# Performance work log

Hardware: AMD Instinct MI355X
Metric: run time of the kernel (lower is better)

Reference implementation:

```python
import jax, jax.numpy as jnp
import numpy as np


def setup_inputs() -> dict:
    key = jax.random.key(0)
    k0, k1, k2, k3, k4 = jax.random.split(key, 5)
    B, H, Lq, Lk, D = 2, 8, 512, 512, 32
    q = jax.random.normal(k0, (B, H, Lq, D), dtype=jnp.float32)
    k = jax.random.normal(k1, (B, H, Lk, D), dtype=jnp.float32)
    scale = jnp.ones((1,), dtype=jnp.float32)  # accepted but unused by the module
    # mask True = padded / excluded (torch masked_fill semantics)
    mask = jax.random.bernoulli(k2, 0.1, (B, Lq, Lk))
    attn_bias = jax.random.normal(k3, (B, H, Lq, Lk), dtype=jnp.float32) * 0.1
    # GATv2 attention vector, torch shape (1,H,1,1,D) -> stored as (H,D)
    limit = float(np.sqrt(6.0 / (1.0 + D)))  # xavier_uniform fan_in=1*1*D? torch uses full shape; scale is immaterial for correctness
    attention = jax.random.uniform(k4, (H, D), dtype=jnp.float32, minval=-limit, maxval=limit)
    return {"q": q, "k": k, "scale": scale, "mask": mask, "attn_bias": attn_bias, "attention": attention}


def reference(q, k, scale, mask, attn_bias, attention):
    # q: [B,H,Lq,D], k: [B,H,Lk,D], attention: [H,D]
    # broadcast additive combine -> [B,H,Lq,Lk,D]
    summed = q[:, :, :, None, :] + k[:, :, None, :, :]
    # SiLU activation, dot with per-head attention vector, reduce D -> [B,H,Lq,Lk]
    scores = jnp.einsum("bhqkd,hd->bhqk", jax.nn.silu(summed), attention)
    scores = scores + attn_bias
    # masked softmax over Lk; mask broadcasts over heads (unsqueeze at -3)
    scores = jnp.where(mask[:, None, :, :], -jnp.inf, scores)
    w = jax.nn.softmax(scores, axis=-1)
    # rows that are fully masked produce NaN -> replace with 0 (torch nan_to_num)
    return jnp.nan_to_num(w, nan=0.0)
```

## Files before the change

### kernel.cpp

```cpp
#include <hip/hip_runtime.h>
#include <hip/hip_bf16.h>
#include <math.h>

#define BB 2
#define HH 8
#define LQ 512
#define LK 512
#define DD 32

#define LOG2E 1.44269504088896f

static __device__ __forceinline__ float fast_rcp(float x) {
#if __has_builtin(__builtin_amdgcn_rcpf)
  return __builtin_amdgcn_rcpf(x);
#else
  return 1.0f / x;
#endif
}

static __device__ __forceinline__ float fast_exp2(float x) {
#if __has_builtin(__builtin_amdgcn_exp2f)
  return __builtin_amdgcn_exp2f(x);
#else
  return __expf(x * 0.69314718056f);
#endif
}


__global__ __launch_bounds__(256) void gatv2_prek_t(
    const float* __restrict__ k, const float* __restrict__ att,
    float2* __restrict__ ktab) {
  const int bh = blockIdx.x >> 3;
  const int kt = blockIdx.x & 7;
  const int h = bh & (HH - 1);
  const int t = threadIdx.x;

  __shared__ float tile[64][33];

  const float4* src = (const float4*)(k + ((size_t)bh * LK + kt * 64) * DD);
#pragma unroll
  for (int i = 0; i < 2; ++i) {
    const int idx = t + i * 256;
    const float4 v = src[idx];
    const int kkl = idx >> 3;
    const int d4 = (idx & 7) * 4;
    tile[kkl][d4 + 0] = v.x; tile[kkl][d4 + 1] = v.y;
    tile[kkl][d4 + 2] = v.z; tile[kkl][d4 + 3] = v.w;
  }
  __syncthreads();

  const int d = t >> 3;
  const int kl0 = (t & 7) * 8;
  const float a = att[h * DD + d];
  float2* dst = ktab + ((size_t)bh * DD + d) * LK + kt * 64 + kl0;
#pragma unroll
  for (int j = 0; j < 8; ++j) {
    const float kv = tile[kl0 + j][d];
    float2 o;
    o.x = fast_exp2(-kv * LOG2E);
    o.y = kv * a;
    dst[j] = o;
  }
}

__global__ __launch_bounds__(256) void gatv2_prek_q(
    const float* __restrict__ q, const float* __restrict__ att,
    float2* __restrict__ qtab) {
  const int idx = blockIdx.x * 256 + threadIdx.x;
  const int row = idx >> 5;
  const int d = idx & 31;
  const int h = (row >> 9) & (HH - 1);
  const float qd = q[idx];
  const float ad = att[h * DD + d];
  float2 c;
  c.x = fast_exp2(-qd * LOG2E);
  c.y = qd * ad;
  qtab[idx] = c;
}

__global__ __launch_bounds__(256) void gatv2_score(
    const float2* __restrict__ ktab, const float2* __restrict__ qtab,
    const float* __restrict__ bias, const int* __restrict__ mask,
    float* __restrict__ scores) {
  const int lane = threadIdx.x & 63;
  const int w = threadIdx.x >> 6;
  const int bid = blockIdx.x;
  const int bh = bid >> 6;
  const int rem = bid & 63;
  const int rg = rem >> 1;
  const int ch = rem & 1;
  const int col = ch * 256 + w * 64 + lane;
  const int row0 = bh * LQ + rg * 16;
  const int b = bh >> 3;

  const float2* __restrict__ kcol = ktab + (size_t)bh * (DD * LK) + col;
  float2 kf[DD];
#pragma unroll
  for (int d = 0; d < DD; ++d) kf[d] = kcol[(size_t)d * LK];

#pragma unroll 2
  for (int rr = 0; rr < 16; ++rr) {
    const int row = row0 + rr;
    const float2* __restrict__ qrow = qtab + (size_t)row * DD;
    float acc = 0.0f;
#pragma unroll
    for (int d = 0; d < DD; ++d) {
      const float2 qc = qrow[d];
      const float u = fmaf(qc.x, kf[d].x, 1.0f);
      const float t = qc.y + kf[d].y;
      acc = fmaf(t, fast_rcp(u), acc);
    }
    const int qi = row & (LQ - 1);
    const float bval = bias[(size_t)row * LK + col];
    const int mval = mask[((size_t)(b * LQ + qi)) * LK + col];
    scores[(size_t)row * LK + col] = mval ? -INFINITY : (acc + bval);
  }
}

__global__ __launch_bounds__(256) void gatv2_softmax(
    const float* __restrict__ scores, float* __restrict__ out) {
  const int lane = threadIdx.x & 63;
  const int wid = threadIdx.x >> 6;
  const int r = blockIdx.x * 4 + wid;

  const float* __restrict__ srow = scores + (size_t)r * LK;
  float sc[8];
#pragma unroll
  for (int c = 0; c < 8; ++c) sc[c] = srow[lane + 64 * c];

  float m = sc[0];
#pragma unroll
  for (int c = 1; c < 8; ++c) m = fmaxf(m, sc[c]);
#pragma unroll
  for (int off = 32; off > 0; off >>= 1)
    m = fmaxf(m, __shfl_xor(m, off, 64));

  float sum = 0.0f;
#pragma unroll
  for (int c = 0; c < 8; ++c) {
    const float p = fast_exp2((sc[c] - m) * LOG2E);
    sc[c] = p;
    sum += p;
  }
#pragma unroll
  for (int off = 32; off > 0; off >>= 1)
    sum += __shfl_xor(sum, off, 64);

  const bool dead = (m == -INFINITY);
  const float inv = dead ? 0.0f : fast_rcp(sum);

  float* __restrict__ orow = out + (size_t)r * LK;
#pragma unroll
  for (int c = 0; c < 8; ++c) {
    orow[lane + 64 * c] = dead ? 0.0f : sc[c] * inv;
  }
}

#define D2 (DD / 2)
#define C2 2
#define NC (D2 / C2)
#define WAVES 8
#define RPW 2
#define ROWSPB (WAVES * RPW)

__global__ __launch_bounds__(256) void gatv2_prek_p(
    const float* __restrict__ k, const float* __restrict__ att,
    float4* __restrict__ wst4) {
  const int bh = blockIdx.x >> 3;
  const int kt = blockIdx.x & 7;
  const int h = bh & (HH - 1);
  const int t = threadIdx.x;

  __shared__ float tile[64][33];

  const float4* src = (const float4*)(k + ((size_t)bh * LK + kt * 64) * DD);
#pragma unroll
  for (int i = 0; i < 2; ++i) {
    const int idx = t + i * 256;
    const float4 v = src[idx];
    const int kkl = idx >> 3;
    const int d4 = (idx & 7) * 4;
    tile[kkl][d4 + 0] = v.x; tile[kkl][d4 + 1] = v.y;
    tile[kkl][d4 + 2] = v.z; tile[kkl][d4 + 3] = v.w;
  }
  __syncthreads();

  const int d2 = t >> 4;
  const int kl0 = (t & 15) * 4;
  const float a0 = att[h * DD + 2 * d2 + 0];
  const float a1 = att[h * DD + 2 * d2 + 1];
  float4* dst = wst4 + ((size_t)bh * D2 + d2) * LK + kt * 64 + kl0;
#pragma unroll
  for (int j = 0; j < 4; ++j) {
    const float k0 = tile[kl0 + j][2 * d2 + 0];
    const float k1 = tile[kl0 + j][2 * d2 + 1];
    float4 o;
    o.x = fast_exp2(-k0 * LOG2E); o.y = k0 * a0;
    o.z = fast_exp2(-k1 * LOG2E); o.w = k1 * a1;
    dst[j] = o;
  }
}

__global__ __launch_bounds__(512) void gatv2_main_r2(
    const float* __restrict__ q, const int* __restrict__ mask,
    const float* __restrict__ bias, const float* __restrict__ att,
    const float4* __restrict__ wst4, float* __restrict__ out) {
  const int lane = threadIdx.x & 63;
  const int wid = threadIdx.x >> 6;
  const int tid = threadIdx.x;
  const int rowbase = blockIdx.x * ROWSPB;
  const int bh = rowbase >> 9;
  const int b = rowbase >> 12;
  const int h = bh & (HH - 1);

  __shared__ float4 lds4[2][C2 * LK];
  __shared__ float4 cst4[ROWSPB][D2];

  const float4* __restrict__ kb = wst4 + (size_t)bh * (D2 * LK);

  float4 s0 = kb[tid];
  float4 s1 = kb[tid + 512];

  {
    const int rw = wid * RPW + (lane >> 5);
    const int d = lane & 31;
    const float qd = q[(size_t)(rowbase + rw) * DD + d];
    const float ad = att[h * DD + d];
    float2 c;
    c.x = fast_exp2(-qd * LOG2E);
    c.y = qd * ad;
    ((float2*)cst4)[rw * DD + d] = c;
  }
  lds4[0][tid] = s0;
  lds4[0][tid + 512] = s1;

  float acc[RPW][8];
#pragma unroll
  for (int j = 0; j < RPW; ++j)
#pragma unroll
    for (int c = 0; c < 8; ++c) acc[j][c] = 0.0f;

  float bv[RPW][8];
  int mv[RPW][8];

#pragma unroll
  for (int cc = 0; cc < NC; ++cc) {
    __syncthreads();

    float4 s0n, s1n;
    if (cc + 1 < NC) {
      const float4* src = kb + (size_t)(cc + 1) * (C2 * LK);
      s0n = src[tid];
      s1n = src[tid + 512];
    } else {
      const float* __restrict__ brow = bias + (size_t)rowbase * LK;
      const int* __restrict__ mrow = mask + ((size_t)(b * LQ) + (rowbase & (LQ - 1))) * LK;
#pragma unroll
      for (int j = 0; j < RPW; ++j) {
        const int rw = wid * RPW + j;
#pragma unroll
        for (int c = 0; c < 8; ++c) {
          bv[j][c] = brow[(size_t)rw * LK + lane + 64 * c];
          mv[j][c] = mrow[(size_t)rw * LK + lane + 64 * c];
        }
      }
    }

    const float4 c0A = cst4[wid * RPW + 0][cc * 2 + 0];
    const float4 c0B = cst4[wid * RPW + 0][cc * 2 + 1];
    const float4 c1A = cst4[wid * RPW + 1][cc * 2 + 0];
    const float4 c1B = cst4[wid * RPW + 1][cc * 2 + 1];

    const float4* __restrict__ buf = lds4[cc & 1];
#pragma unroll
    for (int d2l = 0; d2l < C2; ++d2l) {
      const float4 k0 = d2l ? c0B : c0A;
      const float4 k1 = d2l ? c1B : c1A;
      const float4* __restrict__ pd = buf + d2l * LK + lane;
#pragma unroll
      for (int c = 0; c < 8; ++c) {
        const float4 p = pd[64 * c];
        float u = fmaf(k0.x, p.x, 1.0f);
        float t = k0.y + p.y;
        acc[0][c] = fmaf(t, fast_rcp(u), acc[0][c]);
        u = fmaf(k0.z, p.z, 1.0f);
        t = k0.w + p.w;
        acc[0][c] = fmaf(t, fast_rcp(u), acc[0][c]);
        u = fmaf(k1.x, p.x, 1.0f);
        t = k1.y + p.y;
        acc[1][c] = fmaf(t, fast_rcp(u), acc[1][c]);
        u = fmaf(k1.z, p.z, 1.0f);
        t = k1.w + p.w;
        acc[1][c] = fmaf(t, fast_rcp(u), acc[1][c]);
      }
    }

    if (cc + 1 < NC) {
      float4* dst = lds4[(cc + 1) & 1];
      dst[tid] = s0n;
      dst[tid + 512] = s1n;
    }
  }

#pragma unroll
  for (int j = 0; j < RPW; ++j) {
    const int r = rowbase + wid * RPW + j;

    float sc[8];
#pragma unroll
    for (int c = 0; c < 8; ++c)
      sc[c] = mv[j][c] ? -INFINITY : (acc[j][c] + bv[j][c]);

    float m = sc[0];
#pragma unroll
    for (int c = 1; c < 8; ++c) m = fmaxf(m, sc[c]);
#pragma unroll
    for (int off = 32; off > 0; off >>= 1)
      m = fmaxf(m, __shfl_xor(m, off, 64));

    float sum = 0.0f;
#pragma unroll
    for (int c = 0; c < 8; ++c) {
      const float p = fast_exp2((sc[c] - m) * LOG2E);
      sc[c] = p;
      sum += p;
    }
#pragma unroll
    for (int off = 32; off > 0; off >>= 1)
      sum += __shfl_xor(sum, off, 64);

    const bool dead = (m == -INFINITY);
    const float inv = dead ? 0.0f : fast_rcp(sum);

    float* __restrict__ orow = out + (size_t)r * LK;
#pragma unroll
    for (int c = 0; c < 8; ++c) {
      orow[lane + 64 * c] = dead ? 0.0f : sc[c] * inv;
    }
  }
}

__global__ __launch_bounds__(256) void gatv2_fallback(
    const float* __restrict__ q, const float* __restrict__ k,
    const int* __restrict__ mask, const float* __restrict__ bias,
    const float* __restrict__ att, float* __restrict__ out) {
  const int lane = threadIdx.x & 63;
  const int wid = threadIdx.x >> 6;
  const int r = blockIdx.x * 4 + wid;
  const int b = r >> 12;
  const int h = (r >> 9) & (HH - 1);
  const int qi = r & (LQ - 1);

  const float* __restrict__ qrow = q + (size_t)r * DD;
  const float* __restrict__ kbase = k + ((size_t)(b * HH + h)) * (size_t)(LK * DD);
  const float* __restrict__ arow = att + h * DD;
  const float* __restrict__ brow = bias + (size_t)r * LK;
  const int* __restrict__ mrow = mask + ((size_t)(b * LQ + qi)) * LK;

  float qv[DD], av[DD];
#pragma unroll
  for (int d0 = 0; d0 < DD; d0 += 4) {
    const float4 qq = *(const float4*)(qrow + d0);
    const float4 aa = *(const float4*)(arow + d0);
    qv[d0 + 0] = qq.x; qv[d0 + 1] = qq.y; qv[d0 + 2] = qq.z; qv[d0 + 3] = qq.w;
    av[d0 + 0] = aa.x; av[d0 + 1] = aa.y; av[d0 + 2] = aa.z; av[d0 + 3] = aa.w;
  }

  float sc[8];
#pragma unroll
  for (int c = 0; c < 8; ++c) {
    const int kk = lane + 64 * c;
    const float* __restrict__ kr = kbase + (size_t)kk * DD;
    const float bval = brow[kk];
    const int mval = mrow[kk];
    float acc = 0.0f;
#pragma unroll
    for (int d0 = 0; d0 < DD; d0 += 4) {
      const float4 kv = *(const float4*)(kr + d0);
      const float kvf[4] = {kv.x, kv.y, kv.z, kv.w};
#pragma unroll
      for (int j = 0; j < 4; ++j) {
        const float t = qv[d0 + j] + kvf[j];
        const float e = fast_exp2(t * -LOG2E);
        const float sg = fast_rcp(1.0f + e);
        acc = fmaf(t * sg, av[d0 + j], acc);
      }
    }
    const float s = acc + bval;
    sc[c] = mval ? -INFINITY : s;
  }

  float m = sc[0];
#pragma unroll
  for (int c = 1; c < 8; ++c) m = fmaxf(m, sc[c]);
#pragma unroll
  for (int off = 32; off > 0; off >>= 1)
    m = fmaxf(m, __shfl_xor(m, off, 64));

  float sum = 0.0f;
#pragma unroll
  for (int c = 0; c < 8; ++c) {
    const float p = fast_exp2((sc[c] - m) * LOG2E);
    sc[c] = p;
    sum += p;
  }
#pragma unroll
  for (int off = 32; off > 0; off >>= 1)
    sum += __shfl_xor(sum, off, 64);

  const bool dead = (m == -INFINITY);
  const float inv = dead ? 0.0f : fast_rcp(sum);

  float* __restrict__ orow = out + (size_t)r * LK;
#pragma unroll
  for (int c = 0; c < 8; ++c) {
    orow[lane + 64 * c] = dead ? 0.0f : sc[c] * inv;
  }
}

extern "C" void kernel_launch(void* const* d_in, const int* in_sizes, int n_in,
                              void* d_out, int out_size, void* d_ws, size_t ws_size,
                              hipStream_t stream) {
  const float* q = (const float*)d_in[0];
  const float* k = (const float*)d_in[1];
  const int* mask = (const int*)d_in[3];
  const float* bias = (const float*)d_in[4];
  const float* att = (const float*)d_in[5];
  float* out = (float*)d_out;

  const int rows = BB * HH * LQ;
  const size_t ktab_b = (size_t)BB * HH * DD * LK * sizeof(float2);
  const size_t qtab_b = (size_t)rows * DD * sizeof(float2);
  const size_t scores_b = (size_t)rows * LK * sizeof(float);

  if (ws_size >= ktab_b + qtab_b + scores_b) {
    char* wsb = (char*)d_ws;
    float2* ktab = (float2*)wsb;
    float2* qtab = (float2*)(wsb + ktab_b);
    float* scores = (float*)(wsb + ktab_b + qtab_b);

    gatv2_prek_t<<<dim3(128), dim3(256), 0, stream>>>(k, att, ktab);
    gatv2_prek_q<<<dim3(1024), dim3(256), 0, stream>>>(q, att, qtab);
    gatv2_score<<<dim3(1024), dim3(256), 0, stream>>>(ktab, qtab, bias, mask, scores);
    gatv2_softmax<<<dim3(rows / 4), dim3(256), 0, stream>>>(scores, out);
  } else if (ws_size >= (size_t)BB * HH * D2 * LK * sizeof(float4)) {
    float4* wst4 = (float4*)d_ws;
    gatv2_prek_p<<<dim3(128), dim3(256), 0, stream>>>(k, att, wst4);
    gatv2_main_r2<<<dim3(rows / ROWSPB), dim3(64 * WAVES), 0, stream>>>(
        q, mask, bias, att, wst4, out);
  } else {
    gatv2_fallback<<<dim3(rows / 4), dim3(256), 0, stream>>>(q, k, mask, bias, att, out);
  }
}
```

Before: 116.6 us.

## Fuse score computation and masked softmax into one kernel

Merges the score and softmax kernels. Each 512-thread block covers all 512 key columns for 8 query rows and does the softmax in place, combining per-wave max and sum through shared memory. This removes the write and re-read of the intermediate scores buffer and one kernel launch. In exchange each block reloads the full key table for only 8 rows, where the old kernel reused it across 16, and the larger per-thread register arrays may lower occupancy.

New measurement: 116.9 us. Within noise of the previous version (+0.2%).

```diff
diff --git a/kernel.cpp b/kernel.cpp
--- a/kernel.cpp
+++ b/kernel.cpp
@@ -7,6 +7,7 @@
 #define LQ 512
 #define LK 512
 #define DD 32
+#define RB 8
 
 #define LOG2E 1.44269504088896f
 
@@ -78,29 +79,29 @@
   qtab[idx] = c;
 }
 
-__global__ __launch_bounds__(256) void gatv2_score(
+__global__ __launch_bounds__(512) void gatv2_fused(
     const float2* __restrict__ ktab, const float2* __restrict__ qtab,
     const float* __restrict__ bias, const int* __restrict__ mask,
-    float* __restrict__ scores) {
+    float* __restrict__ out) {
   const int lane = threadIdx.x & 63;
   const int w = threadIdx.x >> 6;
-  const int bid = blockIdx.x;
-  const int bh = bid >> 6;
-  const int rem = bid & 63;
-  const int rg = rem >> 1;
-  const int ch = rem & 1;
-  const int col = ch * 256 + w * 64 + lane;
-  const int row0 = bh * LQ + rg * 16;
+  const int bh = blockIdx.x >> 6;
+  const int rg = blockIdx.x & 63;
+  const int rowbase = bh * LQ + rg * RB;
   const int b = bh >> 3;
+  const int col = w * 64 + lane;
+
+  __shared__ float2 red[RB][8];
 
   const float2* __restrict__ kcol = ktab + (size_t)bh * (DD * LK) + col;
   float2 kf[DD];
 #pragma unroll
   for (int d = 0; d < DD; ++d) kf[d] = kcol[(size_t)d * LK];
 
-#pragma unroll 2
-  for (int rr = 0; rr < 16; ++rr) {
-    const int row = row0 + rr;
+  float sc[RB];
+#pragma unroll
+  for (int rr = 0; rr < RB; ++rr) {
+    const int row = rowbase + rr;
     const float2* __restrict__ qrow = qtab + (size_t)row * DD;
     float acc = 0.0f;
 #pragma unroll
@@ -110,49 +111,52 @@
       const float t = qc.y + kf[d].y;
       acc = fmaf(t, fast_rcp(u), acc);
     }
-    const int qi = row & (LQ - 1);
     const float bval = bias[(size_t)row * LK + col];
-    const int mval = mask[((size_t)(b * LQ + qi)) * LK + col];
-    scores[(size_t)row * LK + col] = mval ? -INFINITY : (acc + bval);
-  }
-}
-
-__global__ __launch_bounds__(256) void gatv2_softmax(
-    const float* __restrict__ scores, float* __restrict__ out) {
-  const int lane = threadIdx.x & 63;
-  const int wid = threadIdx.x >> 6;
-  const int r = blockIdx.x * 4 + wid;
-
-  const float* __restrict__ srow = scores + (size_t)r * LK;
-  float sc[8];
-#pragma unroll
-  for (int c = 0; c < 8; ++c) sc[c] = srow[lane + 64 * c];
-
-  float m = sc[0];
-#pragma unroll
-  for (int c = 1; c < 8; ++c) m = fmaxf(m, sc[c]);
-#pragma unroll
-  for (int off = 32; off > 0; off >>= 1)
-    m = fmaxf(m, __shfl_xor(m, off, 64));
-
-  float sum = 0.0f;
-#pragma unroll
-  for (int c = 0; c < 8; ++c) {
-    const float p = fast_exp2((sc[c] - m) * LOG2E);
-    sc[c] = p;
-    sum += p;
-  }
-#pragma unroll
-  for (int off = 32; off > 0; off >>= 1)
-    sum += __shfl_xor(sum, off, 64);
-
-  const bool dead = (m == -INFINITY);
-  const float inv = dead ? 0.0f : fast_rcp(sum);
-
-  float* __restrict__ orow = out + (size_t)r * LK;
-#pragma unroll
-  for (int c = 0; c < 8; ++c) {
-    orow[lane + 64 * c] = dead ? 0.0f : sc[c] * inv;
+    const int mval = mask[((size_t)(b * LQ + (row & (LQ - 1)))) * LK + col];
+    sc[rr] = mval ? -INFINITY : (acc + bval);
+  }
+
+#pragma unroll
+  for (int rr = 0; rr < RB; ++rr) {
+    float m = sc[rr];
+#pragma unroll
+    for (int off = 32; off > 0; off >>= 1)
+      m = fmaxf(m, __shfl_xor(m, off, 64));
+    const float mws = (m == -INFINITY) ? 0.0f : m;
+    const float p = (sc[rr] == -INFINITY) ? 0.0f
+                                          : fast_exp2((sc[rr] - mws) * LOG2E);
+    float s = p;
+#pragma unroll
+    for (int off = 32; off > 0; off >>= 1)
+      s += __shfl_xor(s, off, 64);
+    if (lane == 0) red[rr][w] = make_float2(m, s);
+    sc[rr] = p;
+  }
+  __syncthreads();
+
+#pragma unroll
+  for (int rr = 0; rr < RB; ++rr) {
+    const int row = rowbase + rr;
+    float2 r0 = red[rr][0], r1 = red[rr][1], r2 = red[rr][2], r3 = red[rr][3];
+    float2 r4 = red[rr][4], r5 = red[rr][5], r6 = red[rr][6], r7 = red[rr][7];
+    float M = fmaxf(fmaxf(fmaxf(r0.x, r1.x), fmaxf(r2.x, r3.x)),
+                    fmaxf(fmaxf(r4.x, r5.x), fmaxf(r6.x, r7.x)));
+    const bool dead = (M == -INFINITY);
+    const float Ms = dead ? 0.0f : M;
+    float S = 0.0f;
+    S += r0.y * ((r0.x == -INFINITY) ? 0.0f : fast_exp2((r0.x - Ms) * LOG2E));
+    S += r1.y * ((r1.x == -INFINITY) ? 0.0f : fast_exp2((r1.x - Ms) * LOG2E));
+    S += r2.y * ((r2.x == -INFINITY) ? 0.0f : fast_exp2((r2.x - Ms) * LOG2E));
+    S += r3.y * ((r3.x == -INFINITY) ? 0.0f : fast_exp2((r3.x - Ms) * LOG2E));
+    S += r4.y * ((r4.x == -INFINITY) ? 0.0f : fast_exp2((r4.x - Ms) * LOG2E));
+    S += r5.y * ((r5.x == -INFINITY) ? 0.0f : fast_exp2((r5.x - Ms) * LOG2E));
+    S += r6.y * ((r6.x == -INFINITY) ? 0.0f : fast_exp2((r6.x - Ms) * LOG2E));
+    S += r7.y * ((r7.x == -INFINITY) ? 0.0f : fast_exp2((r7.x - Ms) * LOG2E));
+
+    const float mw = red[rr][w].x;
+    const float ew = (mw == -INFINITY) ? 0.0f : fast_exp2((mw - Ms) * LOG2E);
+    const float val = sc[rr] * ew * fast_rcp(S);
+    out[(size_t)row * LK + col] = dead ? 0.0f : val;
   }
 }
 
@@ -431,18 +435,15 @@
   const int rows = BB * HH * LQ;
   const size_t ktab_b = (size_t)BB * HH * DD * LK * sizeof(float2);
   const size_t qtab_b = (size_t)rows * DD * sizeof(float2);
-  const size_t scores_b = (size_t)rows * LK * sizeof(float);
-
-  if (ws_size >= ktab_b + qtab_b + scores_b) {
+
+  if (ws_size >= ktab_b + qtab_b) {
     char* wsb = (char*)d_ws;
     float2* ktab = (float2*)wsb;
     float2* qtab = (float2*)(wsb + ktab_b);
-    float* scores = (float*)(wsb + ktab_b + qtab_b);
 
     gatv2_prek_t<<<dim3(128), dim3(256), 0, stream>>>(k, att, ktab);
     gatv2_prek_q<<<dim3(1024), dim3(256), 0, stream>>>(q, att, qtab);
-    gatv2_score<<<dim3(1024), dim3(256), 0, stream>>>(ktab, qtab, bias, mask, scores);
-    gatv2_softmax<<<dim3(rows / 4), dim3(256), 0, stream>>>(scores, out);
+    gatv2_fused<<<dim3(1024), dim3(512), 0, stream>>>(ktab, qtab, bias, mask, out);
   } else if (ws_size >= (size_t)BB * HH * D2 * LK * sizeof(float4)) {
     float4* wst4 = (float4*)d_ws;
     gatv2_prek_p<<<dim3(128), dim3(256), 0, stream>>>(k, att, wst4);
```
